# Kernel optimization log

Measured on AMD Instinct MI355X. Metric: run time of the kernel, lower is better.

The kernel has to match this reference:

```python
import jax, jax.numpy as jnp
import numpy as np

N_NODES = 40000
N_EDGES = 640000
NFEAT = 256
NHID = 128


def setup_inputs() -> dict:
    key = jax.random.key(0)
    k1, k2, k3, k4 = jax.random.split(key, 4)
    x = jax.random.normal(k1, (N_NODES, NFEAT), dtype=jnp.float32)
    edge_index = jax.random.randint(k2, (2, N_EDGES), 0, N_NODES, dtype=jnp.int64)
    edge_weight = jax.random.uniform(k3, (N_EDGES,), dtype=jnp.float32)
    # Glorot-style init for the GraphConvolution weight, zero bias
    W = jax.random.normal(k4, (NFEAT, NHID), dtype=jnp.float32) * (1.0 / np.sqrt(NFEAT))
    b = jnp.zeros((NHID,), dtype=jnp.float32)
    return {"x": x, "edge_index": edge_index, "edge_weight": edge_weight, "W": W, "b": b}


def reference(x, edge_index, edge_weight, W, b):
    # GraphConvolution: support = x @ W ; out = spmm(adj, support) + b ; relu
    support = x @ W                                   # [N, nhid]
    src, dst = edge_index[0], edge_index[1]
    msgs = support[src] * edge_weight[:, None]        # [E, nhid] gathered messages
    agg = jax.ops.segment_sum(msgs, dst, num_segments=N_NODES)  # [N, nhid]
    return jax.nn.relu(agg + b)
```

## Files before the change

kernel.cpp:

```cpp
#include <hip/hip_runtime.h>

#define NNODES 40000
#define NEDGES 640000
#define NFEAT  256
#define NHID   128
#define CAP    48

#define SUP_OFF 0u
#define CUR_OFF 10240000u
#define WT_OFF  10400000u
#define BKT_OFF 10465536u
#define WS_NEEDED (BKT_OFF + (size_t)NNODES * CAP * 8)

typedef float floatx4 __attribute__((ext_vector_type(4)));
typedef __bf16 bf16x8 __attribute__((ext_vector_type(8)));
typedef unsigned short ushort8 __attribute__((ext_vector_type(8)));
union BfFrag { ushort8 s; bf16x8 b; };

__device__ __forceinline__ unsigned short f2bf(float f) {
    unsigned int u = __float_as_uint(f);
    u = (u + 0x7FFFu + ((u >> 16) & 1u)) >> 16;
    return (unsigned short)u;
}

__global__ __launch_bounds__(256) void setup_wt_cur(const float* __restrict__ W,
                                                    unsigned short* __restrict__ Wt,
                                                    int* __restrict__ cursor) {
    const int i = blockIdx.x * 256 + threadIdx.x;
    if (i < NFEAT * NHID) {
        const int h = i >> 8;
        const int k = i & 255;
        Wt[i] = f2bf(W[k * NHID + h]);
    }
    if (i < NNODES) cursor[i] = 0;
}

__global__ __launch_bounds__(256) void gemm_mfma(const float* __restrict__ x,
                                                 const unsigned short* __restrict__ Wt,
                                                 unsigned short* __restrict__ support) {
    const int tid  = threadIdx.x;
    const int lane = tid & 63;
    const int wv   = tid >> 6;
    const int m    = lane & 15;
    const int quad = lane >> 4;
    const int node = blockIdx.x * 64 + wv * 16 + m;

    BfFrag afrag[8];
    const float* xrow = x + (size_t)node * NFEAT + quad * 8;
    #pragma unroll
    for (int ks = 0; ks < 8; ks++) {
        float4 f0 = *(const float4*)(xrow + ks * 32);
        float4 f1 = *(const float4*)(xrow + ks * 32 + 4);
        afrag[ks].s[0] = f2bf(f0.x); afrag[ks].s[1] = f2bf(f0.y);
        afrag[ks].s[2] = f2bf(f0.z); afrag[ks].s[3] = f2bf(f0.w);
        afrag[ks].s[4] = f2bf(f1.x); afrag[ks].s[5] = f2bf(f1.y);
        afrag[ks].s[6] = f2bf(f1.z); afrag[ks].s[7] = f2bf(f1.w);
    }

    floatx4 acc[8];
    #pragma unroll
    for (int nt = 0; nt < 8; nt++) acc[nt] = (floatx4){0.f, 0.f, 0.f, 0.f};

    #pragma unroll
    for (int nt = 0; nt < 8; nt++) {
        const unsigned short* wrow = Wt + (size_t)(nt * 16 + m) * NFEAT + quad * 8;
        #pragma unroll
        for (int ks = 0; ks < 8; ks++) {
            BfFrag bfrag;
            bfrag.s = *(const ushort8*)(wrow + ks * 32);
            acc[nt] = __builtin_amdgcn_mfma_f32_16x16x32_bf16(afrag[ks].b, bfrag.b,
                                                              acc[nt], 0, 0, 0);
        }
    }

    const int row0 = blockIdx.x * 64 + wv * 16 + quad * 4;
    #pragma unroll
    for (int nt = 0; nt < 8; nt++) {
        #pragma unroll
        for (int r = 0; r < 4; r++) {
            support[(size_t)(row0 + r) * NHID + nt * 16 + m] = f2bf(acc[nt][r]);
        }
    }
}

__global__ __launch_bounds__(256) void fill_buckets(const int* __restrict__ ei,
                                                    const float* __restrict__ ew,
                                                    int* __restrict__ cursor,
                                                    int2* __restrict__ bucket) {
    const int e   = blockIdx.x * 256 + threadIdx.x;
    const int dst = ei[NEDGES + e];
    const int pos = atomicAdd(&cursor[dst], 1);
    if (pos < CAP)
        bucket[(size_t)dst * CAP + pos] = make_int2(ei[e], __float_as_int(ew[e]));
}

__device__ __forceinline__ float2 bf2f2(unsigned int u) {
    float2 v;
    v.x = __uint_as_float(u << 16);
    v.y = __uint_as_float(u & 0xFFFF0000u);
    return v;
}

__global__ __launch_bounds__(256) void gather_csr(const int* __restrict__ cursor,
                                                  const int2* __restrict__ bucket,
                                                  const unsigned short* __restrict__ support,
                                                  const float* __restrict__ b,
                                                  float* __restrict__ out) {
    const int node = blockIdx.x * 4 + (threadIdx.x >> 6);
    const int lane = threadIdx.x & 63;

    int cnt = cursor[node];
    if (cnt > CAP) cnt = CAP;
    const int2* bkt = bucket + (size_t)node * CAP;

    const unsigned int* s4 = (const unsigned int*)support;
    float2 a0 = make_float2(0.f, 0.f), a1 = a0, a2 = a0, a3 = a0;

    int i = 0;
    for (; i + 4 <= cnt; i += 4) {
        int2 e0 = bkt[i + 0];
        int2 e1 = bkt[i + 1];
        int2 e2 = bkt[i + 2];
        int2 e3 = bkt[i + 3];
        unsigned int u0 = s4[(size_t)e0.x * (NHID / 2) + lane];
        unsigned int u1 = s4[(size_t)e1.x * (NHID / 2) + lane];
        unsigned int u2 = s4[(size_t)e2.x * (NHID / 2) + lane];
        unsigned int u3 = s4[(size_t)e3.x * (NHID / 2) + lane];
        float w0 = __int_as_float(e0.y), w1 = __int_as_float(e1.y);
        float w2 = __int_as_float(e2.y), w3 = __int_as_float(e3.y);
        float2 v0 = bf2f2(u0), v1 = bf2f2(u1), v2 = bf2f2(u2), v3 = bf2f2(u3);
        a0.x = fmaf(w0, v0.x, a0.x); a0.y = fmaf(w0, v0.y, a0.y);
        a1.x = fmaf(w1, v1.x, a1.x); a1.y = fmaf(w1, v1.y, a1.y);
        a2.x = fmaf(w2, v2.x, a2.x); a2.y = fmaf(w2, v2.y, a2.y);
        a3.x = fmaf(w3, v3.x, a3.x); a3.y = fmaf(w3, v3.y, a3.y);
    }
    for (; i < cnt; ++i) {
        int2 e = bkt[i];
        float w = __int_as_float(e.y);
        float2 v = bf2f2(s4[(size_t)e.x * (NHID / 2) + lane]);
        a0.x = fmaf(w, v.x, a0.x); a0.y = fmaf(w, v.y, a0.y);
    }

    float2 bb = ((const float2*)b)[lane];
    float2 acc;
    acc.x = fmaxf((a0.x + a1.x) + (a2.x + a3.x) + bb.x, 0.f);
    acc.y = fmaxf((a0.y + a1.y) + (a2.y + a3.y) + bb.y, 0.f);
    ((float2*)out)[(size_t)node * (NHID / 2) + lane] = acc;
}

__global__ __launch_bounds__(256) void gemm_xw(const float* __restrict__ x,
                                               const float* __restrict__ W,
                                               float* __restrict__ support) {
    __shared__ float xs[64 * NFEAT];
    const int tid   = threadIdx.x;
    const int node0 = blockIdx.x * 64;

    const float4* xg  = (const float4*)(x + (size_t)node0 * NFEAT);
    float4*       xs4 = (float4*)xs;
    #pragma unroll
    for (int i = tid; i < 64 * (NFEAT / 4); i += 256) xs4[i] = xg[i];
    __syncthreads();

    const int hg = tid & 31;
    const int ng = tid >> 5;
    const float4* W4 = (const float4*)W;

    float4 acc[8];
    #pragma unroll
    for (int n = 0; n < 8; n++) acc[n] = make_float4(0.f, 0.f, 0.f, 0.f);

    #pragma unroll 4
    for (int k = 0; k < NFEAT; k++) {
        float4 w = W4[k * (NHID / 4) + hg];
        #pragma unroll
        for (int n = 0; n < 8; n++) {
            float xv = xs[(ng * 8 + n) * NFEAT + k];
            acc[n].x = fmaf(xv, w.x, acc[n].x);
            acc[n].y = fmaf(xv, w.y, acc[n].y);
            acc[n].z = fmaf(xv, w.z, acc[n].z);
            acc[n].w = fmaf(xv, w.w, acc[n].w);
        }
    }

    float4* out4 = (float4*)support;
    #pragma unroll
    for (int n = 0; n < 8; n++)
        out4[(size_t)(node0 + ng * 8 + n) * (NHID / 4) + hg] = acc[n];
}

__global__ __launch_bounds__(256) void scatter_edges(const int* __restrict__ ei,
                                                     const float* __restrict__ ew,
                                                     const float* __restrict__ support,
                                                     float* __restrict__ out) {
    const int tid  = threadIdx.x;
    const int lane = tid & 31;
    const int e    = blockIdx.x * 8 + (tid >> 5);
    const int   src = ei[e];
    const int   dst = ei[NEDGES + e];
    const float w   = ew[e];
    const float4* s4 = (const float4*)support;
    float4 v = s4[(size_t)src * (NHID / 4) + lane];
    float* o = out + (size_t)dst * NHID + lane * 4;
    atomicAdd(o + 0, v.x * w);
    atomicAdd(o + 1, v.y * w);
    atomicAdd(o + 2, v.z * w);
    atomicAdd(o + 3, v.w * w);
}

__global__ __launch_bounds__(256) void finalize(float* __restrict__ out,
                                                const float* __restrict__ b) {
    const int i = blockIdx.x * 256 + threadIdx.x;
    float4*       o4 = (float4*)out;
    const float4* b4 = (const float4*)b;
    float4 v  = o4[i];
    float4 bb = b4[i & 31];
    v.x = fmaxf(v.x + bb.x, 0.f);
    v.y = fmaxf(v.y + bb.y, 0.f);
    v.z = fmaxf(v.z + bb.z, 0.f);
    v.w = fmaxf(v.w + bb.w, 0.f);
    o4[i] = v;
}

extern "C" void kernel_launch(void* const* d_in, const int* in_sizes, int n_in,
                              void* d_out, int out_size, void* d_ws, size_t ws_size,
                              hipStream_t stream) {
    const float* x  = (const float*)d_in[0];
    const int*   ei = (const int*)d_in[1];
    const float* ew = (const float*)d_in[2];
    const float* W  = (const float*)d_in[3];
    const float* b  = (const float*)d_in[4];
    float*       out = (float*)d_out;

    char* ws = (char*)d_ws;

    if (ws_size >= WS_NEEDED) {
        unsigned short* support = (unsigned short*)(ws + SUP_OFF);
        int*            cursor  = (int*)(ws + CUR_OFF);
        unsigned short* Wt      = (unsigned short*)(ws + WT_OFF);
        int2*           bucket  = (int2*)(ws + BKT_OFF);

        setup_wt_cur<<<160, 256, 0, stream>>>(W, Wt, cursor);
        gemm_mfma<<<NNODES / 64, 256, 0, stream>>>(x, Wt, support);
        fill_buckets<<<NEDGES / 256, 256, 0, stream>>>(ei, ew, cursor, bucket);
        gather_csr<<<NNODES / 4, 256, 0, stream>>>(cursor, bucket, support, b, out);
    } else {
        float* support = (float*)(ws + SUP_OFF);
        gemm_xw<<<NNODES / 64, 256, 0, stream>>>(x, W, support);
        hipMemsetAsync(d_out, 0, (size_t)out_size * sizeof(float), stream);
        scatter_edges<<<NEDGES / 8, 256, 0, stream>>>(ei, ew, support, out);
        finalize<<<out_size / 4 / 256, 256, 0, stream>>>(out, b);
    }
}
```

Before: 178.6 us.

## Pack bucket entries to 32 bits and gather two edges per wave

Each bucket entry now packs a 16-bit source index and a bf16 edge weight into one 32-bit word instead of an int2. This halves the scattered bucket writes and reads. The gather kernel splits each wave into two half-waves that handle alternate edges with 8-byte support loads, then combines them with a cross-half shuffle. Zeroing the cursor moves into the GEMM kernel so the weight-cast kernel is simpler. The cost is lower edge-weight precision and a source index that only fits because the node count is below 65536.

```diff
diff --git a/kernel.cpp b/kernel.cpp
--- a/kernel.cpp
+++ b/kernel.cpp
@@ -10,7 +10,7 @@
 #define CUR_OFF 10240000u
 #define WT_OFF  10400000u
 #define BKT_OFF 10465536u
-#define WS_NEEDED (BKT_OFF + (size_t)NNODES * CAP * 8)
+#define WS_NEEDED (BKT_OFF + (size_t)NNODES * CAP * 4)
 
 typedef float floatx4 __attribute__((ext_vector_type(4)));
 typedef __bf16 bf16x8 __attribute__((ext_vector_type(8)));
@@ -23,22 +23,30 @@
     return (unsigned short)u;
 }
 
-__global__ __launch_bounds__(256) void setup_wt_cur(const float* __restrict__ W,
-                                                    unsigned short* __restrict__ Wt,
-                                                    int* __restrict__ cursor) {
+__device__ __forceinline__ float4 bf4(uint2 u) {
+    float4 v;
+    v.x = __uint_as_float(u.x << 16);
+    v.y = __uint_as_float(u.x & 0xFFFF0000u);
+    v.z = __uint_as_float(u.y << 16);
+    v.w = __uint_as_float(u.y & 0xFFFF0000u);
+    return v;
+}
+
+__global__ __launch_bounds__(256) void cast_wt(const float* __restrict__ W,
+                                               unsigned short* __restrict__ Wt) {
     const int i = blockIdx.x * 256 + threadIdx.x;
-    if (i < NFEAT * NHID) {
-        const int h = i >> 8;
-        const int k = i & 255;
-        Wt[i] = f2bf(W[k * NHID + h]);
-    }
-    if (i < NNODES) cursor[i] = 0;
+    const int h = i >> 8;
+    const int k = i & 255;
+    Wt[i] = f2bf(W[k * NHID + h]);
 }
 
 __global__ __launch_bounds__(256) void gemm_mfma(const float* __restrict__ x,
                                                  const unsigned short* __restrict__ Wt,
-                                                 unsigned short* __restrict__ support) {
+                                                 unsigned short* __restrict__ support,
+                                                 int* __restrict__ cursor) {
     const int tid  = threadIdx.x;
+    if (tid < 64) cursor[blockIdx.x * 64 + tid] = 0;
+
     const int lane = tid & 63;
     const int wv   = tid >> 6;
     const int m    = lane & 15;
@@ -86,66 +94,90 @@
 __global__ __launch_bounds__(256) void fill_buckets(const int* __restrict__ ei,
                                                     const float* __restrict__ ew,
                                                     int* __restrict__ cursor,
-                                                    int2* __restrict__ bucket) {
+                                                    unsigned int* __restrict__ bucket) {
     const int e   = blockIdx.x * 256 + threadIdx.x;
+    const int src = ei[e];
     const int dst = ei[NEDGES + e];
+    const unsigned int entry = ((unsigned int)f2bf(ew[e]) << 16) | (unsigned int)src;
     const int pos = atomicAdd(&cursor[dst], 1);
     if (pos < CAP)
-        bucket[(size_t)dst * CAP + pos] = make_int2(ei[e], __float_as_int(ew[e]));
-}
-
-__device__ __forceinline__ float2 bf2f2(unsigned int u) {
-    float2 v;
-    v.x = __uint_as_float(u << 16);
-    v.y = __uint_as_float(u & 0xFFFF0000u);
-    return v;
+        bucket[(size_t)dst * CAP + pos] = entry;
 }
 
 __global__ __launch_bounds__(256) void gather_csr(const int* __restrict__ cursor,
-                                                  const int2* __restrict__ bucket,
+                                                  const unsigned int* __restrict__ bucket,
                                                   const unsigned short* __restrict__ support,
                                                   const float* __restrict__ b,
                                                   float* __restrict__ out) {
     const int node = blockIdx.x * 4 + (threadIdx.x >> 6);
     const int lane = threadIdx.x & 63;
+    const int h    = lane >> 5;
+    const int hl   = lane & 31;
 
     int cnt = cursor[node];
     if (cnt > CAP) cnt = CAP;
-    const int2* bkt = bucket + (size_t)node * CAP;
-
-    const unsigned int* s4 = (const unsigned int*)support;
-    float2 a0 = make_float2(0.f, 0.f), a1 = a0, a2 = a0, a3 = a0;
+    const unsigned int* bkt   = bucket + (size_t)node * CAP;
+    const uint2*        sup2  = (const uint2*)support;
+
+    float4 a0 = make_float4(0.f, 0.f, 0.f, 0.f), a1 = a0, a2 = a0, a3 = a0;
 
     int i = 0;
-    for (; i + 4 <= cnt; i += 4) {
-        int2 e0 = bkt[i + 0];
-        int2 e1 = bkt[i + 1];
-        int2 e2 = bkt[i + 2];
-        int2 e3 = bkt[i + 3];
-        unsigned int u0 = s4[(size_t)e0.x * (NHID / 2) + lane];
-        unsigned int u1 = s4[(size_t)e1.x * (NHID / 2) + lane];
-        unsigned int u2 = s4[(size_t)e2.x * (NHID / 2) + lane];
-        unsigned int u3 = s4[(size_t)e3.x * (NHID / 2) + lane];
-        float w0 = __int_as_float(e0.y), w1 = __int_as_float(e1.y);
-        float w2 = __int_as_float(e2.y), w3 = __int_as_float(e3.y);
-        float2 v0 = bf2f2(u0), v1 = bf2f2(u1), v2 = bf2f2(u2), v3 = bf2f2(u3);
+    for (; i + 8 <= cnt; i += 8) {
+        unsigned int e0 = bkt[i + 0 + h];
+        unsigned int e1 = bkt[i + 2 + h];
+        unsigned int e2 = bkt[i + 4 + h];
+        unsigned int e3 = bkt[i + 6 + h];
+        uint2 u0 = sup2[(size_t)(e0 & 0xFFFFu) * 32 + hl];
+        uint2 u1 = sup2[(size_t)(e1 & 0xFFFFu) * 32 + hl];
+        uint2 u2 = sup2[(size_t)(e2 & 0xFFFFu) * 32 + hl];
+        uint2 u3 = sup2[(size_t)(e3 & 0xFFFFu) * 32 + hl];
+        float w0 = __uint_as_float(e0 & 0xFFFF0000u);
+        float w1 = __uint_as_float(e1 & 0xFFFF0000u);
+        float w2 = __uint_as_float(e2 & 0xFFFF0000u);
+        float w3 = __uint_as_float(e3 & 0xFFFF0000u);
+        float4 v0 = bf4(u0), v1 = bf4(u1), v2 = bf4(u2), v3 = bf4(u3);
         a0.x = fmaf(w0, v0.x, a0.x); a0.y = fmaf(w0, v0.y, a0.y);
+        a0.z = fmaf(w0, v0.z, a0.z); a0.w = fmaf(w0, v0.w, a0.w);
         a1.x = fmaf(w1, v1.x, a1.x); a1.y = fmaf(w1, v1.y, a1.y);
+        a1.z = fmaf(w1, v1.z, a1.z); a1.w = fmaf(w1, v1.w, a1.w);
         a2.x = fmaf(w2, v2.x, a2.x); a2.y = fmaf(w2, v2.y, a2.y);
+        a2.z = fmaf(w2, v2.z, a2.z); a2.w = fmaf(w2, v2.w, a2.w);
         a3.x = fmaf(w3, v3.x, a3.x); a3.y = fmaf(w3, v3.y, a3.y);
-    }
-    for (; i < cnt; ++i) {
-        int2 e = bkt[i];
-        float w = __int_as_float(e.y);
-        float2 v = bf2f2(s4[(size_t)e.x * (NHID / 2) + lane]);
-        a0.x = fmaf(w, v.x, a0.x); a0.y = fmaf(w, v.y, a0.y);
-    }
-
-    float2 bb = ((const float2*)b)[lane];
-    float2 acc;
-    acc.x = fmaxf((a0.x + a1.x) + (a2.x + a3.x) + bb.x, 0.f);
-    acc.y = fmaxf((a0.y + a1.y) + (a2.y + a3.y) + bb.y, 0.f);
-    ((float2*)out)[(size_t)node * (NHID / 2) + lane] = acc;
+        a3.z = fmaf(w3, v3.z, a3.z); a3.w = fmaf(w3, v3.w, a3.w);
+    }
+
+    if (i < cnt) {
+        #pragma unroll
+        for (int j = 0; j < 4; j++) {
+            int e = i + 2 * j + h;
+            bool valid = e < cnt;
+            unsigned int ent = bkt[valid ? e : (cnt - 1)];
+            float w = valid ? __uint_as_float(ent & 0xFFFF0000u) : 0.f;
+            uint2 u = sup2[(size_t)(ent & 0xFFFFu) * 32 + hl];
+            float4 v = bf4(u);
+            a0.x = fmaf(w, v.x, a0.x); a0.y = fmaf(w, v.y, a0.y);
+            a0.z = fmaf(w, v.z, a0.z); a0.w = fmaf(w, v.w, a0.w);
+        }
+    }
+
+    float4 a;
+    a.x = (a0.x + a1.x) + (a2.x + a3.x);
+    a.y = (a0.y + a1.y) + (a2.y + a3.y);
+    a.z = (a0.z + a1.z) + (a2.z + a3.z);
+    a.w = (a0.w + a1.w) + (a2.w + a3.w);
+    a.x += __shfl_xor(a.x, 32);
+    a.y += __shfl_xor(a.y, 32);
+    a.z += __shfl_xor(a.z, 32);
+    a.w += __shfl_xor(a.w, 32);
+
+    if (h == 0) {
+        float4 bb = ((const float4*)b)[hl];
+        a.x = fmaxf(a.x + bb.x, 0.f);
+        a.y = fmaxf(a.y + bb.y, 0.f);
+        a.z = fmaxf(a.z + bb.z, 0.f);
+        a.w = fmaxf(a.w + bb.w, 0.f);
+        ((float4*)out)[(size_t)node * (NHID / 4) + hl] = a;
+    }
 }
 
 __global__ __launch_bounds__(256) void gemm_xw(const float* __restrict__ x,
@@ -237,10 +269,10 @@
         unsigned short* support = (unsigned short*)(ws + SUP_OFF);
         int*            cursor  = (int*)(ws + CUR_OFF);
         unsigned short* Wt      = (unsigned short*)(ws + WT_OFF);
-        int2*           bucket  = (int2*)(ws + BKT_OFF);
-
-        setup_wt_cur<<<160, 256, 0, stream>>>(W, Wt, cursor);
-        gemm_mfma<<<NNODES / 64, 256, 0, stream>>>(x, Wt, support);
+        unsigned int*   bucket  = (unsigned int*)(ws + BKT_OFF);
+
+        cast_wt<<<(NFEAT * NHID) / 256, 256, 0, stream>>>(W, Wt);
+        gemm_mfma<<<NNODES / 64, 256, 0, stream>>>(x, Wt, support, cursor);
         fill_buckets<<<NEDGES / 256, 256, 0, stream>>>(ei, ew, cursor, bucket);
         gather_csr<<<NNODES / 4, 256, 0, stream>>>(cursor, bucket, support, b, out);
     } else {
```

Measured after the change: 169.8 us. 1.05x faster.

## Fuse GEMM with bucket fill, pack bucket entries to 32 bits, widen gather loads

Applied to the files above, without the earlier changes.

Merges the MFMA GEMM and the edge bucket-fill into one launch, with extra blocks doing the fill, so the two can overlap and one launch is saved. Each bucket entry shrinks from 8 to 4 bytes by packing a 16-bit source index with a bf16 edge weight. The gather now has each quarter-wave process a different edge with 16-byte support loads, then combines the quarters with shuffles. This relies on node count fitting in 16 bits and lowers edge-weight precision to bf16.

```diff
diff --git a/kernel.cpp b/kernel.cpp
--- a/kernel.cpp
+++ b/kernel.cpp
@@ -10,7 +10,10 @@
 #define CUR_OFF 10240000u
 #define WT_OFF  10400000u
 #define BKT_OFF 10465536u
-#define WS_NEEDED (BKT_OFF + (size_t)NNODES * CAP * 8)
+#define WS_NEEDED (BKT_OFF + (size_t)NNODES * CAP * 4)
+
+#define GEMM_BLOCKS (NNODES / 64)
+#define FILL_BLOCKS (NEDGES / 256)
 
 typedef float floatx4 __attribute__((ext_vector_type(4)));
 typedef __bf16 bf16x8 __attribute__((ext_vector_type(8)));
@@ -21,6 +24,15 @@
     unsigned int u = __float_as_uint(f);
     u = (u + 0x7FFFu + ((u >> 16) & 1u)) >> 16;
     return (unsigned short)u;
+}
+
+__device__ __forceinline__ float4 bf4(unsigned int lo, unsigned int hi) {
+    float4 v;
+    v.x = __uint_as_float(lo << 16);
+    v.y = __uint_as_float(lo & 0xFFFF0000u);
+    v.z = __uint_as_float(hi << 16);
+    v.w = __uint_as_float(hi & 0xFFFF0000u);
+    return v;
 }
 
 __global__ __launch_bounds__(256) void setup_wt_cur(const float* __restrict__ W,
@@ -35,10 +47,26 @@
     if (i < NNODES) cursor[i] = 0;
 }
 
-__global__ __launch_bounds__(256) void gemm_mfma(const float* __restrict__ x,
+__global__ __launch_bounds__(256) void gemm_fill(const float* __restrict__ x,
                                                  const unsigned short* __restrict__ Wt,
-                                                 unsigned short* __restrict__ support) {
-    const int tid  = threadIdx.x;
+                                                 unsigned short* __restrict__ support,
+                                                 const int* __restrict__ ei,
+                                                 const float* __restrict__ ew,
+                                                 int* __restrict__ cursor,
+                                                 unsigned int* __restrict__ bucket) {
+    const int tid = threadIdx.x;
+
+    if (blockIdx.x >= GEMM_BLOCKS) {
+        const int e   = (blockIdx.x - GEMM_BLOCKS) * 256 + tid;
+        const int src = ei[e];
+        const int dst = ei[NEDGES + e];
+        const unsigned int entry = ((unsigned int)f2bf(ew[e]) << 16) | (unsigned int)src;
+        const int pos = atomicAdd(&cursor[dst], 1);
+        if (pos < CAP)
+            bucket[(size_t)dst * CAP + pos] = entry;
+        return;
+    }
+
     const int lane = tid & 63;
     const int wv   = tid >> 6;
     const int m    = lane & 15;
@@ -83,69 +111,106 @@
     }
 }
 
-__global__ __launch_bounds__(256) void fill_buckets(const int* __restrict__ ei,
-                                                    const float* __restrict__ ew,
-                                                    int* __restrict__ cursor,
-                                                    int2* __restrict__ bucket) {
-    const int e   = blockIdx.x * 256 + threadIdx.x;
-    const int dst = ei[NEDGES + e];
-    const int pos = atomicAdd(&cursor[dst], 1);
-    if (pos < CAP)
-        bucket[(size_t)dst * CAP + pos] = make_int2(ei[e], __float_as_int(ew[e]));
-}
-
-__device__ __forceinline__ float2 bf2f2(unsigned int u) {
-    float2 v;
-    v.x = __uint_as_float(u << 16);
-    v.y = __uint_as_float(u & 0xFFFF0000u);
-    return v;
-}
-
 __global__ __launch_bounds__(256) void gather_csr(const int* __restrict__ cursor,
-                                                  const int2* __restrict__ bucket,
+                                                  const unsigned int* __restrict__ bucket,
                                                   const unsigned short* __restrict__ support,
                                                   const float* __restrict__ b,
                                                   float* __restrict__ out) {
     const int node = blockIdx.x * 4 + (threadIdx.x >> 6);
     const int lane = threadIdx.x & 63;
+    const int q    = lane >> 4;
+    const int ql   = lane & 15;
 
     int cnt = cursor[node];
     if (cnt > CAP) cnt = CAP;
-    const int2* bkt = bucket + (size_t)node * CAP;
-
-    const unsigned int* s4 = (const unsigned int*)support;
-    float2 a0 = make_float2(0.f, 0.f), a1 = a0, a2 = a0, a3 = a0;
+    const unsigned int* bkt  = bucket + (size_t)node * CAP;
+    const uint4*        sup4 = (const uint4*)support;
+
+    float4 lo0 = make_float4(0.f, 0.f, 0.f, 0.f), lo1 = lo0, lo2 = lo0, lo3 = lo0;
+    float4 hi0 = lo0, hi1 = lo0, hi2 = lo0, hi3 = lo0;
 
     int i = 0;
-    for (; i + 4 <= cnt; i += 4) {
-        int2 e0 = bkt[i + 0];
-        int2 e1 = bkt[i + 1];
-        int2 e2 = bkt[i + 2];
-        int2 e3 = bkt[i + 3];
-        unsigned int u0 = s4[(size_t)e0.x * (NHID / 2) + lane];
-        unsigned int u1 = s4[(size_t)e1.x * (NHID / 2) + lane];
-        unsigned int u2 = s4[(size_t)e2.x * (NHID / 2) + lane];
-        unsigned int u3 = s4[(size_t)e3.x * (NHID / 2) + lane];
-        float w0 = __int_as_float(e0.y), w1 = __int_as_float(e1.y);
-        float w2 = __int_as_float(e2.y), w3 = __int_as_float(e3.y);
-        float2 v0 = bf2f2(u0), v1 = bf2f2(u1), v2 = bf2f2(u2), v3 = bf2f2(u3);
-        a0.x = fmaf(w0, v0.x, a0.x); a0.y = fmaf(w0, v0.y, a0.y);
-        a1.x = fmaf(w1, v1.x, a1.x); a1.y = fmaf(w1, v1.y, a1.y);
-        a2.x = fmaf(w2, v2.x, a2.x); a2.y = fmaf(w2, v2.y, a2.y);
-        a3.x = fmaf(w3, v3.x, a3.x); a3.y = fmaf(w3, v3.y, a3.y);
-    }
-    for (; i < cnt; ++i) {
-        int2 e = bkt[i];
-        float w = __int_as_float(e.y);
-        float2 v = bf2f2(s4[(size_t)e.x * (NHID / 2) + lane]);
-        a0.x = fmaf(w, v.x, a0.x); a0.y = fmaf(w, v.y, a0.y);
-    }
-
-    float2 bb = ((const float2*)b)[lane];
-    float2 acc;
-    acc.x = fmaxf((a0.x + a1.x) + (a2.x + a3.x) + bb.x, 0.f);
-    acc.y = fmaxf((a0.y + a1.y) + (a2.y + a3.y) + bb.y, 0.f);
-    ((float2*)out)[(size_t)node * (NHID / 2) + lane] = acc;
+    for (; i + 16 <= cnt; i += 16) {
+        unsigned int e0 = bkt[i + 0  + q];
+        unsigned int e1 = bkt[i + 4  + q];
+        unsigned int e2 = bkt[i + 8  + q];
+        unsigned int e3 = bkt[i + 12 + q];
+        uint4 u0 = sup4[(size_t)(e0 & 0xFFFFu) * 16 + ql];
+        uint4 u1 = sup4[(size_t)(e1 & 0xFFFFu) * 16 + ql];
+        uint4 u2 = sup4[(size_t)(e2 & 0xFFFFu) * 16 + ql];
+        uint4 u3 = sup4[(size_t)(e3 & 0xFFFFu) * 16 + ql];
+        float w0 = __uint_as_float(e0 & 0xFFFF0000u);
+        float w1 = __uint_as_float(e1 & 0xFFFF0000u);
+        float w2 = __uint_as_float(e2 & 0xFFFF0000u);
+        float w3 = __uint_as_float(e3 & 0xFFFF0000u);
+        float4 vl0 = bf4(u0.x, u0.y), vh0 = bf4(u0.z, u0.w);
+        float4 vl1 = bf4(u1.x, u1.y), vh1 = bf4(u1.z, u1.w);
+        float4 vl2 = bf4(u2.x, u2.y), vh2 = bf4(u2.z, u2.w);
+        float4 vl3 = bf4(u3.x, u3.y), vh3 = bf4(u3.z, u3.w);
+        lo0.x = fmaf(w0, vl0.x, lo0.x); lo0.y = fmaf(w0, vl0.y, lo0.y);
+        lo0.z = fmaf(w0, vl0.z, lo0.z); lo0.w = fmaf(w0, vl0.w, lo0.w);
+        hi0.x = fmaf(w0, vh0.x, hi0.x); hi0.y = fmaf(w0, vh0.y, hi0.y);
+        hi0.z = fmaf(w0, vh0.z, hi0.z); hi0.w = fmaf(w0, vh0.w, hi0.w);
+        lo1.x = fmaf(w1, vl1.x, lo1.x); lo1.y = fmaf(w1, vl1.y, lo1.y);
+        lo1.z = fmaf(w1, vl1.z, lo1.z); lo1.w = fmaf(w1, vl1.w, lo1.w);
+        hi1.x = fmaf(w1, vh1.x, hi1.x); hi1.y = fmaf(w1, vh1.y, hi1.y);
+        hi1.z = fmaf(w1, vh1.z, hi1.z); hi1.w = fmaf(w1, vh1.w, hi1.w);
+        lo2.x = fmaf(w2, vl2.x, lo2.x); lo2.y = fmaf(w2, vl2.y, lo2.y);
+        lo2.z = fmaf(w2, vl2.z, lo2.z); lo2.w = fmaf(w2, vl2.w, lo2.w);
+        hi2.x = fmaf(w2, vh2.x, hi2.x); hi2.y = fmaf(w2, vh2.y, hi2.y);
+        hi2.z = fmaf(w2, vh2.z, hi2.z); hi2.w = fmaf(w2, vh2.w, hi2.w);
+        lo3.x = fmaf(w3, vl3.x, lo3.x); lo3.y = fmaf(w3, vl3.y, lo3.y);
+        lo3.z = fmaf(w3, vl3.z, lo3.z); lo3.w = fmaf(w3, vl3.w, lo3.w);
+        hi3.x = fmaf(w3, vh3.x, hi3.x); hi3.y = fmaf(w3, vh3.y, hi3.y);
+        hi3.z = fmaf(w3, vh3.z, hi3.z); hi3.w = fmaf(w3, vh3.w, hi3.w);
+    }
+
+    if (i < cnt) {
+        #pragma unroll
+        for (int j = 0; j < 4; j++) {
+            int e = i + 4 * j + q;
+            bool valid = e < cnt;
+            unsigned int ent = bkt[valid ? e : 0];
+            float w = valid ? __uint_as_float(ent & 0xFFFF0000u) : 0.f;
+            uint4 u = sup4[(size_t)(ent & 0xFFFFu) * 16 + ql];
+            float4 vl = bf4(u.x, u.y), vh = bf4(u.z, u.w);
+            lo0.x = fmaf(w, vl.x, lo0.x); lo0.y = fmaf(w, vl.y, lo0.y);
+            lo0.z = fmaf(w, vl.z, lo0.z); lo0.w = fmaf(w, vl.w, lo0.w);
+            hi0.x = fmaf(w, vh.x, hi0.x); hi0.y = fmaf(w, vh.y, hi0.y);
+            hi0.z = fmaf(w, vh.z, hi0.z); hi0.w = fmaf(w, vh.w, hi0.w);
+        }
+    }
+
+    float4 L, H;
+    L.x = (lo0.x + lo1.x) + (lo2.x + lo3.x);
+    L.y = (lo0.y + lo1.y) + (lo2.y + lo3.y);
+    L.z = (lo0.z + lo1.z) + (lo2.z + lo3.z);
+    L.w = (lo0.w + lo1.w) + (lo2.w + lo3.w);
+    H.x = (hi0.x + hi1.x) + (hi2.x + hi3.x);
+    H.y = (hi0.y + hi1.y) + (hi2.y + hi3.y);
+    H.z = (hi0.z + hi1.z) + (hi2.z + hi3.z);
+    H.w = (hi0.w + hi1.w) + (hi2.w + hi3.w);
+
+    L.x += __shfl_xor(L.x, 16); L.y += __shfl_xor(L.y, 16);
+    L.z += __shfl_xor(L.z, 16); L.w += __shfl_xor(L.w, 16);
+    H.x += __shfl_xor(H.x, 16); H.y += __shfl_xor(H.y, 16);
+    H.z += __shfl_xor(H.z, 16); H.w += __shfl_xor(H.w, 16);
+    L.x += __shfl_xor(L.x, 32); L.y += __shfl_xor(L.y, 32);
+    L.z += __shfl_xor(L.z, 32); L.w += __shfl_xor(L.w, 32);
+    H.x += __shfl_xor(H.x, 32); H.y += __shfl_xor(H.y, 32);
+    H.z += __shfl_xor(H.z, 32); H.w += __shfl_xor(H.w, 32);
+
+    if (q == 0) {
+        const float4* b4p = (const float4*)b;
+        float4 bl = b4p[ql * 2], bh = b4p[ql * 2 + 1];
+        L.x = fmaxf(L.x + bl.x, 0.f); L.y = fmaxf(L.y + bl.y, 0.f);
+        L.z = fmaxf(L.z + bl.z, 0.f); L.w = fmaxf(L.w + bl.w, 0.f);
+        H.x = fmaxf(H.x + bh.x, 0.f); H.y = fmaxf(H.y + bh.y, 0.f);
+        H.z = fmaxf(H.z + bh.z, 0.f); H.w = fmaxf(H.w + bh.w, 0.f);
+        float4* o4 = (float4*)out + (size_t)node * (NHID / 4);
+        o4[ql * 2]     = L;
+        o4[ql * 2 + 1] = H;
+    }
 }
 
 __global__ __launch_bounds__(256) void gemm_xw(const float* __restrict__ x,
@@ -237,11 +302,11 @@
         unsigned short* support = (unsigned short*)(ws + SUP_OFF);
         int*            cursor  = (int*)(ws + CUR_OFF);
         unsigned short* Wt      = (unsigned short*)(ws + WT_OFF);
-        int2*           bucket  = (int2*)(ws + BKT_OFF);
+        unsigned int*   bucket  = (unsigned int*)(ws + BKT_OFF);
 
         setup_wt_cur<<<160, 256, 0, stream>>>(W, Wt, cursor);
-        gemm_mfma<<<NNODES / 64, 256, 0, stream>>>(x, Wt, support);
-        fill_buckets<<<NEDGES / 256, 256, 0, stream>>>(ei, ew, cursor, bucket);
+        gemm_fill<<<GEMM_BLOCKS + FILL_BLOCKS, 256, 0, stream>>>(
+            x, Wt, support, ei, ew, cursor, bucket);
         gather_csr<<<NNODES / 4, 256, 0, stream>>>(cursor, bucket, support, b, out);
     } else {
         float* support = (float*)(ws + SUP_OFF);
```

Result: faster. 164.8 us (-7.8%).
